# Kernel tuning notes

Hardware: AMD Instinct MI355X
Metric: run time of the kernel (lower is better)

The kernel has to match this reference:

```python
import jax, jax.numpy as jnp
import numpy as np

D_H, HEAD, LAYER_IDX = 1024, 16, 11
D_ATTN = D_H // HEAD
BZ, LEN = 2, 2048


def setup_inputs() -> dict:
    key = jax.random.key(0)
    ks = jax.random.split(key, 8)
    s = 1.0 / np.sqrt(D_H)
    v = jax.random.normal(ks[0], (BZ, LEN, D_H), jnp.float32)
    k = jax.random.normal(ks[1], (BZ, LEN, D_H), jnp.float32)
    q = jax.random.normal(ks[2], (BZ, LEN, D_H), jnp.float32)
    # causal mask: 1.0 where attention is blocked (j > i)
    causal = jnp.triu(jnp.ones((LEN, LEN), jnp.float32), k=1)
    mask = jnp.broadcast_to(causal[None, None], (BZ, 1, LEN, LEN))
    Wv = jax.random.normal(ks[3], (D_H, D_H), jnp.float32) * s
    Wk = jax.random.normal(ks[4], (D_H, D_H), jnp.float32) * s
    Wq = jax.random.normal(ks[5], (D_H, D_H), jnp.float32) * s
    Wo = jax.random.normal(ks[6], (D_H, D_H), jnp.float32) * s
    bo = jnp.zeros((D_H,), jnp.float32)
    return {"v": v, "k": k, "q": q, "mask": mask,
            "Wv": Wv, "Wk": Wk, "Wq": Wq, "Wo": Wo, "bo": bo}


def _split_head(x):
    # (bz, len, d_h) -> (bz, head, len, d_attn)
    bz, L, _ = x.shape
    return x.reshape(bz, L, HEAD, D_ATTN).transpose(0, 2, 1, 3)


def reference(v, k, q, mask, Wv, Wk, Wq, Wo, bo):
    bz, len_q, _ = q.shape
    vh = _split_head(v @ Wv)  # (bz, head, len_k, d_attn)
    kh = _split_head(k @ Wk)
    qh = _split_head(q @ Wq)
    scale = 1.0 / jnp.sqrt(jnp.asarray(D_ATTN, jnp.float32))
    weight = jnp.einsum("bhqd,bhkd->bhqk", qh, kh) * scale
    weight = weight + mask * (-1e9)
    weight = weight / jnp.asarray(LAYER_IDX + 1, jnp.float32)
    attn = jax.nn.softmax(weight, axis=-1)  # dropout omitted (inference)
    out = jnp.einsum("bhqk,bhkd->bhqd", attn, vh)
    out = out.transpose(0, 2, 1, 3).reshape(bz, len_q, D_H)
    return out @ Wo + bo
```

## Files before the change

### kernel.cpp

```cpp
#include <hip/hip_runtime.h>
#include <hip/hip_fp16.h>

typedef _Float16 f16;
typedef _Float16 f16x4 __attribute__((ext_vector_type(4)));
typedef _Float16 f16x8 __attribute__((ext_vector_type(8)));
typedef float f32x4 __attribute__((ext_vector_type(4)));

#define D_H   1024
#define LEN   2048
#define BZ    2
#define NHEAD 16
#define DA    64
#define MTOK  (BZ * LEN)
#define KDIM  1024
#define ATT_SCALE (0.125f / 12.0f)

__device__ __forceinline__ void load_lds16(const f16* g, f16* l) {
  __builtin_amdgcn_global_load_lds((const __attribute__((address_space(1))) void*)g,
                                   (__attribute__((address_space(3))) void*)l,
                                   16, 0, 0);
}

__global__ __launch_bounds__(256)
void k_convert3(const float* __restrict__ q, const float* __restrict__ k,
                const float* __restrict__ v, f16* __restrict__ q16,
                f16* __restrict__ k16, f16* __restrict__ v16) {
  const float* in = (blockIdx.y == 0) ? q : (blockIdx.y == 1) ? k : v;
  f16* out = (blockIdx.y == 0) ? q16 : (blockIdx.y == 1) ? k16 : v16;
  int i = (blockIdx.x * 256 + threadIdx.x) * 4;
  float4 x = *(const float4*)(in + i);
  f16x4 o; o[0] = (f16)x.x; o[1] = (f16)x.y; o[2] = (f16)x.z; o[3] = (f16)x.w;
  *(f16x4*)(out + i) = o;
}

__global__ __launch_bounds__(256)
void k_transpose4(const float* __restrict__ W0, const float* __restrict__ W1,
                  const float* __restrict__ W2, const float* __restrict__ W3,
                  f16* __restrict__ T0, f16* __restrict__ T1,
                  f16* __restrict__ T2, f16* __restrict__ T3) {
  int z = blockIdx.z;
  const float* W = (z == 0) ? W0 : (z == 1) ? W1 : (z == 2) ? W2 : W3;
  f16* Wt = (z == 0) ? T0 : (z == 1) ? T1 : (z == 2) ? T2 : T3;
  __shared__ float tile[32][33];
  int bx = blockIdx.x, by = blockIdx.y;
  int tx = threadIdx.x, ty = threadIdx.y;
#pragma unroll
  for (int s = 0; s < 4; ++s)
    tile[ty + 8 * s][tx] = W[(size_t)(by * 32 + ty + 8 * s) * D_H + bx * 32 + tx];
  __syncthreads();
#pragma unroll
  for (int s = 0; s < 4; ++s)
    Wt[(size_t)(bx * 32 + ty + 8 * s) * D_H + by * 32 + tx] =
        (f16)tile[tx][ty + 8 * s];
}

#define BM 128
#define BN 128
#define BK 64
__device__ __forceinline__ void gemm_core(const f16* __restrict__ A,
                                          const f16* __restrict__ Bt,
                                          f16* As, f16* Bs,
                                          f32x4 (&acc)[4][4]) {
  const int tid = threadIdx.x;
  const int wave = tid >> 6, lane = tid & 63;
  const int lc = lane & 15, quad = lane >> 4;
  const int wm = (wave >> 1) * 64, wn = (wave & 1) * 64;
  const int swz = lc & 7;

  for (int k0 = 0; k0 < KDIM; k0 += BK) {
#pragma unroll
    for (int r = 0; r < 4; ++r) {
      int idx = tid + r * 256;
      int row = idx >> 3, ch = idx & 7;
      int gch = ch ^ (row & 7);
      load_lds16(A + (size_t)row * KDIM + k0 + gch * 8, &As[idx * 8]);
    }
#pragma unroll
    for (int r = 0; r < 4; ++r) {
      int idx = tid + r * 256;
      int row = idx >> 3, ch = idx & 7;
      int gch = ch ^ (row & 7);
      load_lds16(Bt + (size_t)row * KDIM + k0 + gch * 8, &Bs[idx * 8]);
    }
    __syncthreads();
#pragma unroll
    for (int kc = 0; kc < 2; ++kc) {
      f16x8 af[4], bf[4];
#pragma unroll
      for (int mi = 0; mi < 4; ++mi)
        af[mi] = *(const f16x8*)&As[(wm + mi * 16 + lc) * 64 +
                                    (((kc * 4 + quad) ^ swz) * 8)];
#pragma unroll
      for (int ni = 0; ni < 4; ++ni)
        bf[ni] = *(const f16x8*)&Bs[(wn + ni * 16 + lc) * 64 +
                                    (((kc * 4 + quad) ^ swz) * 8)];
#pragma unroll
      for (int mi = 0; mi < 4; ++mi)
#pragma unroll
        for (int ni = 0; ni < 4; ++ni)
          acc[mi][ni] = __builtin_amdgcn_mfma_f32_16x16x32_f16(
              af[mi], bf[ni], acc[mi][ni], 0, 0, 0);
    }
    __syncthreads();
  }
}

__global__ __launch_bounds__(256)
void k_gemm3(const f16* __restrict__ A0, const f16* __restrict__ A1,
             const f16* __restrict__ A2, const f16* __restrict__ W0,
             const f16* __restrict__ W1, const f16* __restrict__ W2,
             f16* __restrict__ O0, f16* __restrict__ O1, f16* __restrict__ O2) {
  __shared__ __align__(16) char smem[(BM + BN) * BK * 2];
  f16* As = (f16*)smem;
  f16* Bs = As + BM * BK;
  const int z = blockIdx.z;
  const f16* A = (z == 0) ? A0 : (z == 1) ? A1 : A2;
  const f16* Bt = (z == 0) ? W0 : (z == 1) ? W1 : W2;
  f16* Out = (z == 0) ? O0 : (z == 1) ? O1 : O2;
  const int m0 = blockIdx.x * BM, n0 = blockIdx.y * BN;
  const int tid = threadIdx.x;
  const int wave = tid >> 6, lane = tid & 63;
  const int lc = lane & 15, quad = lane >> 4;
  const int wm = (wave >> 1) * 64;

  f32x4 acc[4][4] = {};
  gemm_core(A + (size_t)m0 * KDIM, Bt + (size_t)n0 * KDIM, As, Bs, acc);

  if (z <= 1) {
    f16* Ct = (f16*)smem;
#pragma unroll
    for (int hf = 0; hf < 2; ++hf) {
      __syncthreads();
      if ((wave & 1) == hf) {
#pragma unroll
        for (int mi = 0; mi < 4; ++mi)
#pragma unroll
          for (int ni = 0; ni < 4; ++ni)
#pragma unroll
            for (int r = 0; r < 4; ++r) {
              int tok = wm + mi * 16 + quad * 4 + r;
              int d = ni * 16 + lc;
              Ct[tok * 72 + d] = (f16)acc[mi][ni][r];
            }
      }
      __syncthreads();
      int hA = (n0 >> 6) + hf;
#pragma unroll
      for (int it = 0; it < 4; ++it) {
        int u = tid + it * 256;
        int tok = u >> 3, ch = u & 7;
        int gm = m0 + tok;
        int b = gm >> 11, i = gm & 2047;
        f16x8 vv = *(const f16x8*)&Ct[tok * 72 + ch * 8];
        *(f16x8*)(Out + ((size_t)((b << 4) + hA) * LEN + i) * DA + ch * 8) = vv;
      }
    }
  } else {
    f16* Ct = (f16*)smem;
    const int b = m0 >> 11, j0m = m0 & 2047;
#pragma unroll
    for (int hf = 0; hf < 2; ++hf) {
      __syncthreads();
      if ((wave & 1) == hf) {
#pragma unroll
        for (int mi = 0; mi < 4; ++mi)
#pragma unroll
          for (int ni = 0; ni < 4; ++ni)
#pragma unroll
            for (int r = 0; r < 4; ++r) {
              int tok = wm + mi * 16 + quad * 4 + r;
              int d = ni * 16 + lc;
              Ct[d * 136 + tok] = (f16)acc[mi][ni][r];
            }
      }
      __syncthreads();
      int hA = (n0 >> 6) + hf;
#pragma unroll
      for (int it = 0; it < 4; ++it) {
        int u = tid + it * 256;
        int d = u >> 4, ch = u & 15;
        f16x8 vv = *(const f16x8*)&Ct[d * 136 + ch * 8];
        *(f16x8*)(Out + ((size_t)((b << 4) + hA) * DA + d) * LEN + j0m + ch * 8) = vv;
      }
    }
  }
}

#define OM 64
#define ON 128
__global__ __launch_bounds__(256)
void k_gemm_out(const f16* __restrict__ A, const f16* __restrict__ Bt,
                float* __restrict__ Out, const float* __restrict__ bias) {
  __shared__ __align__(16) char smem[(OM + ON) * BK * 2];
  f16* As = (f16*)smem;
  f16* Bs = As + OM * BK;
  const int m0 = blockIdx.x * OM, n0 = blockIdx.y * ON;
  const int tid = threadIdx.x;
  const int wave = tid >> 6, lane = tid & 63;
  const int lc = lane & 15, quad = lane >> 4;
  const int wm = (wave >> 1) * 32, wn = (wave & 1) * 64;
  const int swz = lc & 7;

  f32x4 acc[2][4] = {};

  for (int k0 = 0; k0 < KDIM; k0 += BK) {
#pragma unroll
    for (int r = 0; r < 2; ++r) {
      int idx = tid + r * 256;
      int row = idx >> 3, ch = idx & 7;
      int gch = ch ^ (row & 7);
      load_lds16(A + (size_t)(m0 + row) * KDIM + k0 + gch * 8, &As[idx * 8]);
    }
#pragma unroll
    for (int r = 0; r < 4; ++r) {
      int idx = tid + r * 256;
      int row = idx >> 3, ch = idx & 7;
      int gch = ch ^ (row & 7);
      load_lds16(Bt + (size_t)(n0 + row) * KDIM + k0 + gch * 8, &Bs[idx * 8]);
    }
    __syncthreads();
#pragma unroll
    for (int kc = 0; kc < 2; ++kc) {
      f16x8 af[2], bf[4];
#pragma unroll
      for (int mi = 0; mi < 2; ++mi)
        af[mi] = *(const f16x8*)&As[(wm + mi * 16 + lc) * 64 +
                                    (((kc * 4 + quad) ^ swz) * 8)];
#pragma unroll
      for (int ni = 0; ni < 4; ++ni)
        bf[ni] = *(const f16x8*)&Bs[(wn + ni * 16 + lc) * 64 +
                                    (((kc * 4 + quad) ^ swz) * 8)];
#pragma unroll
      for (int mi = 0; mi < 2; ++mi)
#pragma unroll
        for (int ni = 0; ni < 4; ++ni)
          acc[mi][ni] = __builtin_amdgcn_mfma_f32_16x16x32_f16(
              af[mi], bf[ni], acc[mi][ni], 0, 0, 0);
    }
    __syncthreads();
  }

  float* Ct = (float*)smem;
#pragma unroll
  for (int hf = 0; hf < 2; ++hf) {
    __syncthreads();
    if ((wave & 1) == hf) {
#pragma unroll
      for (int mi = 0; mi < 2; ++mi)
#pragma unroll
        for (int ni = 0; ni < 4; ++ni)
#pragma unroll
          for (int r = 0; r < 4; ++r) {
            int tok = wm + mi * 16 + quad * 4 + r;
            int d = ni * 16 + lc;
            Ct[tok * 68 + d] = acc[mi][ni][r];
          }
    }
    __syncthreads();
#pragma unroll
    for (int it = 0; it < 4; ++it) {
      int u = tid + it * 256;
      int tok = u >> 4, ch = u & 15;
      int gm = m0 + tok;
      int gc = n0 + hf * 64 + ch * 4;
      float4 bv = *(const float4*)(bias + gc);
      float4 cv = *(const float4*)&Ct[tok * 68 + ch * 4];
      float4 ov;
      ov.x = cv.x + bv.x; ov.y = cv.y + bv.y;
      ov.z = cv.z + bv.z; ov.w = cv.w + bv.w;
      *(float4*)(Out + (size_t)gm * D_H + gc) = ov;
    }
  }
}

__global__ __launch_bounds__(256, 4)
void k_attn(const f16* __restrict__ Qh, const f16* __restrict__ Kh,
            const f16* __restrict__ Vt, f16* __restrict__ O16) {
  __shared__ f16 Ks[2][64 * 64];
  __shared__ f16 Vs[2][64 * 64];
  __shared__ f16 Pl[4][16 * 64];
  const int tid = threadIdx.x;
  const int wave = tid >> 6, lane = tid & 63;
  const int lc = lane & 15, quad = lane >> 4;
  const int swz = lc & 7;
  const int bh = blockIdx.x & 31;
  const int qb = 31 - (blockIdx.x >> 5);
  const int i0 = qb * 64 + wave * 16;
  const int b = bh >> 4, h = bh & 15;
  const f16* Qb = Qh + (size_t)bh * LEN * DA;
  const f16* Kb = Kh + (size_t)bh * LEN * DA;
  const f16* Vb = Vt + (size_t)bh * DA * LEN;

  f16x8 aQ[2];
#pragma unroll
  for (int c = 0; c < 2; ++c)
    aQ[c] = *(const f16x8*)(Qb + (size_t)(i0 + lc) * DA + c * 32 + quad * 8);

  float lsum[4] = {0.f, 0.f, 0.f, 0.f};
  f32x4 accO[4] = {};
  f16* P = &Pl[wave][0];

  const int niter = qb + 1;

#pragma unroll
  for (int r = 0; r < 2; ++r) {
    int idx = tid + r * 256;
    int row = idx >> 3, ch = idx & 7;
    int gch = ch ^ (row & 7);
    load_lds16(Kb + (size_t)row * DA + gch * 8, &Ks[0][idx * 8]);
  }
#pragma unroll
  for (int r = 0; r < 2; ++r) {
    int idx = tid + r * 256;
    int row = idx >> 3, ch = idx & 7;
    int gch = ch ^ (row & 7);
    load_lds16(Vb + (size_t)row * LEN + gch * 8, &Vs[0][idx * 8]);
  }

  for (int t = 0; t < niter; ++t) {
    __syncthreads();
    if (t + 1 < niter) {
      int j0n = (t + 1) * 64, nb = (t + 1) & 1;
#pragma unroll
      for (int r = 0; r < 2; ++r) {
        int idx = tid + r * 256;
        int row = idx >> 3, ch = idx & 7;
        int gch = ch ^ (row & 7);
        load_lds16(Kb + (size_t)(j0n + row) * DA + gch * 8, &Ks[nb][idx * 8]);
      }
#pragma unroll
      for (int r = 0; r < 2; ++r) {
        int idx = tid + r * 256;
        int row = idx >> 3, ch = idx & 7;
        int gch = ch ^ (row & 7);
        load_lds16(Vb + (size_t)row * LEN + j0n + gch * 8, &Vs[nb][idx * 8]);
      }
    }
    const f16* ks = Ks[t & 1];
    const f16* vs = Vs[t & 1];

    f32x4 s[4] = {};
#pragma unroll
    for (int g = 0; g < 4; ++g)
#pragma unroll
      for (int c = 0; c < 2; ++c) {
        f16x8 bK = *(const f16x8*)&ks[(g * 16 + lc) * 64 +
                                      (((c * 4 + quad) ^ swz) * 8)];
        s[g] = __builtin_amdgcn_mfma_f32_16x16x32_f16(aQ[c], bK, s[g], 0, 0, 0);
      }
    if (t == niter - 1) {
      const int j0 = t * 64;
#pragma unroll
      for (int g = 0; g < 4; ++g)
#pragma unroll
        for (int r = 0; r < 4; ++r) {
          int row = quad * 4 + r;
          int col = g * 16 + lc;
          float e = __expf(s[g][r] * ATT_SCALE);
          e = (j0 + col > i0 + row) ? 0.f : e;
          lsum[r] += e;
          P[(row * 8 + (((col >> 3)) ^ (row & 7))) * 8 + (col & 7)] = (f16)e;
        }
    } else {
#pragma unroll
      for (int g = 0; g < 4; ++g)
#pragma unroll
        for (int r = 0; r < 4; ++r) {
          int row = quad * 4 + r;
          int col = g * 16 + lc;
          float e = __expf(s[g][r] * ATT_SCALE);
          lsum[r] += e;
          P[(row * 8 + (((col >> 3)) ^ (row & 7))) * 8 + (col & 7)] = (f16)e;
        }
    }
    f16x8 aP0 = *(const f16x8*)&P[(lc * 8 + (quad ^ swz)) * 8];
    f16x8 aP1 = *(const f16x8*)&P[(lc * 8 + ((4 + quad) ^ swz)) * 8];
#pragma unroll
    for (int dc = 0; dc < 4; ++dc) {
      f16x8 bV0 = *(const f16x8*)&vs[(dc * 16 + lc) * 64 + ((quad ^ swz) * 8)];
      f16x8 bV1 = *(const f16x8*)&vs[(dc * 16 + lc) * 64 + (((4 + quad) ^ swz) * 8)];
      accO[dc] = __builtin_amdgcn_mfma_f32_16x16x32_f16(aP0, bV0, accO[dc], 0, 0, 0);
      accO[dc] = __builtin_amdgcn_mfma_f32_16x16x32_f16(aP1, bV1, accO[dc], 0, 0, 0);
    }
  }

#pragma unroll
  for (int off = 1; off < 16; off <<= 1)
#pragma unroll
    for (int r = 0; r < 4; ++r) lsum[r] += __shfl_xor(lsum[r], off, 64);

#pragma unroll
  for (int dc = 0; dc < 4; ++dc)
#pragma unroll
    for (int r = 0; r < 4; ++r) {
      int i = i0 + quad * 4 + r;
      int d = dc * 16 + lc;
      float v = accO[dc][r] / lsum[r];
      O16[((size_t)(b * LEN + i)) * D_H + h * DA + d] = (f16)v;
    }
}

extern "C" void kernel_launch(void* const* d_in, const int* in_sizes, int n_in,
                              void* d_out, int out_size, void* d_ws, size_t ws_size,
                              hipStream_t stream) {
  const float* v_f = (const float*)d_in[0];
  const float* k_f = (const float*)d_in[1];
  const float* q_f = (const float*)d_in[2];
  const float* Wv = (const float*)d_in[4];
  const float* Wk = (const float*)d_in[5];
  const float* Wq = (const float*)d_in[6];
  const float* Wo = (const float*)d_in[7];
  const float* bo = (const float*)d_in[8];
  float* out = (float*)d_out;

  const size_t SZ_X = (size_t)MTOK * D_H;
  const size_t SZ_W = (size_t)D_H * D_H;
  f16* ws = (f16*)d_ws;
  f16* q16 = ws;
  f16* k16 = ws + SZ_X;
  f16* v16 = ws + 2 * SZ_X;
  f16* Qh  = ws + 3 * SZ_X;
  f16* Kh  = ws + 4 * SZ_X;
  f16* Vt  = ws + 5 * SZ_X;
  f16* Wqt = ws + 6 * SZ_X;
  f16* Wkt = Wqt + SZ_W;
  f16* Wvt = Wqt + 2 * SZ_W;
  f16* Wot = Wqt + 3 * SZ_W;
  f16* O16 = q16;

  k_convert3<<<dim3((int)(SZ_X / 1024), 3), 256, 0, stream>>>(q_f, k_f, v_f,
                                                              q16, k16, v16);
  k_transpose4<<<dim3(32, 32, 4), dim3(32, 8), 0, stream>>>(
      Wq, Wk, Wv, Wo, Wqt, Wkt, Wvt, Wot);

  k_gemm3<<<dim3(MTOK / BM, D_H / BN, 3), 256, 0, stream>>>(
      q16, k16, v16, Wqt, Wkt, Wvt, Qh, Kh, Vt);

  k_attn<<<dim3(32 * 32), 256, 0, stream>>>(Qh, Kh, Vt, O16);

  k_gemm_out<<<dim3(MTOK / OM, D_H / ON), 256, 0, stream>>>(O16, Wot, out, bo);
}
```

Measured before the change: 228.9 us.

## Fuse fp32-to-fp16 input conversion into QKV GEMM, double-buffer output GEMM, restructure attention

Drops the separate conversion kernel: the QKV projection GEMM now reads fp32 activations directly and converts them to fp16 while storing into LDS. This removes one launch and an extra write and read of three activation tensors, but the A-tile loads are no longer asynchronous direct-to-LDS. The output projection GEMM gains double-buffered LDS staging so the next K-tile loads while the current one computes. The attention kernel pre-scales Q in fp16, computes the transposed score tile so each lane holds one query's row sum, and writes P as packed f16x4. These steps cut per-element scaling, shuffle reductions and scalar LDS stores.

```diff
diff --git a/kernel.cpp b/kernel.cpp
--- a/kernel.cpp
+++ b/kernel.cpp
@@ -19,18 +19,6 @@
   __builtin_amdgcn_global_load_lds((const __attribute__((address_space(1))) void*)g,
                                    (__attribute__((address_space(3))) void*)l,
                                    16, 0, 0);
-}
-
-__global__ __launch_bounds__(256)
-void k_convert3(const float* __restrict__ q, const float* __restrict__ k,
-                const float* __restrict__ v, f16* __restrict__ q16,
-                f16* __restrict__ k16, f16* __restrict__ v16) {
-  const float* in = (blockIdx.y == 0) ? q : (blockIdx.y == 1) ? k : v;
-  f16* out = (blockIdx.y == 0) ? q16 : (blockIdx.y == 1) ? k16 : v16;
-  int i = (blockIdx.x * 256 + threadIdx.x) * 4;
-  float4 x = *(const float4*)(in + i);
-  f16x4 o; o[0] = (f16)x.x; o[1] = (f16)x.y; o[2] = (f16)x.z; o[3] = (f16)x.w;
-  *(f16x4*)(out + i) = o;
 }
 
 __global__ __launch_bounds__(256)
@@ -57,74 +45,71 @@
 #define BM 128
 #define BN 128
 #define BK 64
-__device__ __forceinline__ void gemm_core(const f16* __restrict__ A,
-                                          const f16* __restrict__ Bt,
-                                          f16* As, f16* Bs,
-                                          f32x4 (&acc)[4][4]) {
-  const int tid = threadIdx.x;
-  const int wave = tid >> 6, lane = tid & 63;
-  const int lc = lane & 15, quad = lane >> 4;
-  const int wm = (wave >> 1) * 64, wn = (wave & 1) * 64;
-  const int swz = lc & 7;
-
-  for (int k0 = 0; k0 < KDIM; k0 += BK) {
-#pragma unroll
-    for (int r = 0; r < 4; ++r) {
-      int idx = tid + r * 256;
-      int row = idx >> 3, ch = idx & 7;
-      int gch = ch ^ (row & 7);
-      load_lds16(A + (size_t)row * KDIM + k0 + gch * 8, &As[idx * 8]);
-    }
-#pragma unroll
-    for (int r = 0; r < 4; ++r) {
-      int idx = tid + r * 256;
-      int row = idx >> 3, ch = idx & 7;
-      int gch = ch ^ (row & 7);
-      load_lds16(Bt + (size_t)row * KDIM + k0 + gch * 8, &Bs[idx * 8]);
-    }
-    __syncthreads();
-#pragma unroll
-    for (int kc = 0; kc < 2; ++kc) {
-      f16x8 af[4], bf[4];
-#pragma unroll
-      for (int mi = 0; mi < 4; ++mi)
-        af[mi] = *(const f16x8*)&As[(wm + mi * 16 + lc) * 64 +
-                                    (((kc * 4 + quad) ^ swz) * 8)];
-#pragma unroll
-      for (int ni = 0; ni < 4; ++ni)
-        bf[ni] = *(const f16x8*)&Bs[(wn + ni * 16 + lc) * 64 +
-                                    (((kc * 4 + quad) ^ swz) * 8)];
-#pragma unroll
-      for (int mi = 0; mi < 4; ++mi)
-#pragma unroll
-        for (int ni = 0; ni < 4; ++ni)
-          acc[mi][ni] = __builtin_amdgcn_mfma_f32_16x16x32_f16(
-              af[mi], bf[ni], acc[mi][ni], 0, 0, 0);
-    }
-    __syncthreads();
-  }
-}
-
 __global__ __launch_bounds__(256)
-void k_gemm3(const f16* __restrict__ A0, const f16* __restrict__ A1,
-             const f16* __restrict__ A2, const f16* __restrict__ W0,
+void k_gemm3(const float* __restrict__ A0, const float* __restrict__ A1,
+             const float* __restrict__ A2, const f16* __restrict__ W0,
              const f16* __restrict__ W1, const f16* __restrict__ W2,
              f16* __restrict__ O0, f16* __restrict__ O1, f16* __restrict__ O2) {
   __shared__ __align__(16) char smem[(BM + BN) * BK * 2];
   f16* As = (f16*)smem;
   f16* Bs = As + BM * BK;
   const int z = blockIdx.z;
-  const f16* A = (z == 0) ? A0 : (z == 1) ? A1 : A2;
+  const float* A = (z == 0) ? A0 : (z == 1) ? A1 : A2;
   const f16* Bt = (z == 0) ? W0 : (z == 1) ? W1 : W2;
   f16* Out = (z == 0) ? O0 : (z == 1) ? O1 : O2;
   const int m0 = blockIdx.x * BM, n0 = blockIdx.y * BN;
   const int tid = threadIdx.x;
   const int wave = tid >> 6, lane = tid & 63;
   const int lc = lane & 15, quad = lane >> 4;
-  const int wm = (wave >> 1) * 64;
+  const int wm = (wave >> 1) * 64, wn = (wave & 1) * 64;
+  const int swz = lc & 7;
+  const float* Ab = A + (size_t)m0 * KDIM;
+  const f16* Bb = Bt + (size_t)n0 * KDIM;
 
   f32x4 acc[4][4] = {};
-  gemm_core(A + (size_t)m0 * KDIM, Bt + (size_t)n0 * KDIM, As, Bs, acc);
+
+  for (int k0 = 0; k0 < KDIM; k0 += BK) {
+#pragma unroll
+    for (int r = 0; r < 4; ++r) {
+      int idx = tid + r * 256;
+      int row = idx >> 3, ch = idx & 7;
+      int gch = ch ^ (row & 7);
+      const float* src = Ab + (size_t)row * KDIM + k0 + gch * 8;
+      float4 x0 = *(const float4*)src;
+      float4 x1 = *(const float4*)(src + 4);
+      f16x8 hh;
+      hh[0] = (f16)x0.x; hh[1] = (f16)x0.y; hh[2] = (f16)x0.z; hh[3] = (f16)x0.w;
+      hh[4] = (f16)x1.x; hh[5] = (f16)x1.y; hh[6] = (f16)x1.z; hh[7] = (f16)x1.w;
+      *(f16x8*)&As[idx * 8] = hh;
+    }
+#pragma unroll
+    for (int r = 0; r < 4; ++r) {
+      int idx = tid + r * 256;
+      int row = idx >> 3, ch = idx & 7;
+      int gch = ch ^ (row & 7);
+      load_lds16(Bb + (size_t)row * KDIM + k0 + gch * 8, &Bs[idx * 8]);
+    }
+    __syncthreads();
+#pragma unroll
+    for (int kc = 0; kc < 2; ++kc) {
+      f16x8 af[4], bf[4];
+#pragma unroll
+      for (int mi = 0; mi < 4; ++mi)
+        af[mi] = *(const f16x8*)&As[(wm + mi * 16 + lc) * 64 +
+                                    (((kc * 4 + quad) ^ swz) * 8)];
+#pragma unroll
+      for (int ni = 0; ni < 4; ++ni)
+        bf[ni] = *(const f16x8*)&Bs[(wn + ni * 16 + lc) * 64 +
+                                    (((kc * 4 + quad) ^ swz) * 8)];
+#pragma unroll
+      for (int mi = 0; mi < 4; ++mi)
+#pragma unroll
+        for (int ni = 0; ni < 4; ++ni)
+          acc[mi][ni] = __builtin_amdgcn_mfma_f32_16x16x32_f16(
+              af[mi], bf[ni], acc[mi][ni], 0, 0, 0);
+    }
+    __syncthreads();
+  }
 
   if (z <= 1) {
     f16* Ct = (f16*)smem;
@@ -188,47 +173,61 @@
 
 #define OM 64
 #define ON 128
+#define ONIT (KDIM / BK)
 __global__ __launch_bounds__(256)
 void k_gemm_out(const f16* __restrict__ A, const f16* __restrict__ Bt,
                 float* __restrict__ Out, const float* __restrict__ bias) {
-  __shared__ __align__(16) char smem[(OM + ON) * BK * 2];
+  __shared__ __align__(16) char smem[2 * (OM + ON) * BK * 2];
   f16* As = (f16*)smem;
-  f16* Bs = As + OM * BK;
+  f16* Bs = As + 2 * OM * BK;
   const int m0 = blockIdx.x * OM, n0 = blockIdx.y * ON;
   const int tid = threadIdx.x;
   const int wave = tid >> 6, lane = tid & 63;
   const int lc = lane & 15, quad = lane >> 4;
   const int wm = (wave >> 1) * 32, wn = (wave & 1) * 64;
   const int swz = lc & 7;
+  const f16* Abase = A + (size_t)m0 * KDIM;
+  const f16* Bbase = Bt + (size_t)n0 * KDIM;
 
   f32x4 acc[2][4] = {};
 
-  for (int k0 = 0; k0 < KDIM; k0 += BK) {
-#pragma unroll
-    for (int r = 0; r < 2; ++r) {
-      int idx = tid + r * 256;
-      int row = idx >> 3, ch = idx & 7;
-      int gch = ch ^ (row & 7);
-      load_lds16(A + (size_t)(m0 + row) * KDIM + k0 + gch * 8, &As[idx * 8]);
-    }
-#pragma unroll
-    for (int r = 0; r < 4; ++r) {
-      int idx = tid + r * 256;
-      int row = idx >> 3, ch = idx & 7;
-      int gch = ch ^ (row & 7);
-      load_lds16(Bt + (size_t)(n0 + row) * KDIM + k0 + gch * 8, &Bs[idx * 8]);
-    }
-    __syncthreads();
+#define STAGE_OUT(t)                                                          \
+  {                                                                           \
+    int k0s = (t) * BK;                                                       \
+    f16* Ad = As + ((t) & 1) * (OM * BK);                                     \
+    f16* Bd = Bs + ((t) & 1) * (ON * BK);                                     \
+    _Pragma("unroll")                                                         \
+    for (int r = 0; r < 2; ++r) {                                             \
+      int idx = tid + r * 256;                                                \
+      int row = idx >> 3, ch = idx & 7;                                       \
+      int gch = ch ^ (row & 7);                                               \
+      load_lds16(Abase + (size_t)row * KDIM + k0s + gch * 8, &Ad[idx * 8]);   \
+    }                                                                         \
+    _Pragma("unroll")                                                         \
+    for (int r = 0; r < 4; ++r) {                                             \
+      int idx = tid + r * 256;                                                \
+      int row = idx >> 3, ch = idx & 7;                                       \
+      int gch = ch ^ (row & 7);                                               \
+      load_lds16(Bbase + (size_t)row * KDIM + k0s + gch * 8, &Bd[idx * 8]);   \
+    }                                                                         \
+  }
+
+  STAGE_OUT(0);
+  for (int t = 0; t < ONIT; ++t) {
+    __syncthreads();
+    if (t + 1 < ONIT) STAGE_OUT(t + 1);
+    const f16* Ad = As + (t & 1) * (OM * BK);
+    const f16* Bd = Bs + (t & 1) * (ON * BK);
 #pragma unroll
     for (int kc = 0; kc < 2; ++kc) {
       f16x8 af[2], bf[4];
 #pragma unroll
       for (int mi = 0; mi < 2; ++mi)
-        af[mi] = *(const f16x8*)&As[(wm + mi * 16 + lc) * 64 +
+        af[mi] = *(const f16x8*)&Ad[(wm + mi * 16 + lc) * 64 +
                                     (((kc * 4 + quad) ^ swz) * 8)];
 #pragma unroll
       for (int ni = 0; ni < 4; ++ni)
-        bf[ni] = *(const f16x8*)&Bs[(wn + ni * 16 + lc) * 64 +
+        bf[ni] = *(const f16x8*)&Bd[(wn + ni * 16 + lc) * 64 +
                                     (((kc * 4 + quad) ^ swz) * 8)];
 #pragma unroll
       for (int mi = 0; mi < 2; ++mi)
@@ -237,7 +236,6 @@
           acc[mi][ni] = __builtin_amdgcn_mfma_f32_16x16x32_f16(
               af[mi], bf[ni], acc[mi][ni], 0, 0, 0);
     }
-    __syncthreads();
   }
 
   float* Ct = (float*)smem;
@@ -278,7 +276,7 @@
             const f16* __restrict__ Vt, f16* __restrict__ O16) {
   __shared__ f16 Ks[2][64 * 64];
   __shared__ f16 Vs[2][64 * 64];
-  __shared__ f16 Pl[4][16 * 64];
+  __shared__ f16 Pw[4][16 * 64];
   const int tid = threadIdx.x;
   const int wave = tid >> 6, lane = tid & 63;
   const int lc = lane & 15, quad = lane >> 4;
@@ -292,13 +290,17 @@
   const f16* Vb = Vt + (size_t)bh * DA * LEN;
 
   f16x8 aQ[2];
-#pragma unroll
-  for (int c = 0; c < 2; ++c)
+  const f16 qs = (f16)ATT_SCALE;
+#pragma unroll
+  for (int c = 0; c < 2; ++c) {
     aQ[c] = *(const f16x8*)(Qb + (size_t)(i0 + lc) * DA + c * 32 + quad * 8);
-
-  float lsum[4] = {0.f, 0.f, 0.f, 0.f};
+#pragma unroll
+    for (int j = 0; j < 8; ++j) aQ[c][j] = aQ[c][j] * qs;
+  }
+
+  float lsum = 0.f;
   f32x4 accO[4] = {};
-  f16* P = &Pl[wave][0];
+  f16* P = &Pw[wave][0];
 
   const int niter = qb + 1;
 
@@ -339,55 +341,67 @@
     const f16* ks = Ks[t & 1];
     const f16* vs = Vs[t & 1];
 
-    f32x4 s[4] = {};
+    f32x4 st[4] = {};
 #pragma unroll
     for (int g = 0; g < 4; ++g)
 #pragma unroll
       for (int c = 0; c < 2; ++c) {
-        f16x8 bK = *(const f16x8*)&ks[(g * 16 + lc) * 64 +
+        f16x8 aK = *(const f16x8*)&ks[(g * 16 + lc) * 64 +
                                       (((c * 4 + quad) ^ swz) * 8)];
-        s[g] = __builtin_amdgcn_mfma_f32_16x16x32_f16(aQ[c], bK, s[g], 0, 0, 0);
-      }
+        st[g] = __builtin_amdgcn_mfma_f32_16x16x32_f16(aK, aQ[c], st[g], 0, 0, 0);
+      }
+    float ev[4][4];
     if (t == niter - 1) {
-      const int j0 = t * 64;
+      const int j0 = t * 64, q = i0 + lc;
 #pragma unroll
       for (int g = 0; g < 4; ++g)
 #pragma unroll
         for (int r = 0; r < 4; ++r) {
-          int row = quad * 4 + r;
-          int col = g * 16 + lc;
-          float e = __expf(s[g][r] * ATT_SCALE);
-          e = (j0 + col > i0 + row) ? 0.f : e;
-          lsum[r] += e;
-          P[(row * 8 + (((col >> 3)) ^ (row & 7))) * 8 + (col & 7)] = (f16)e;
+          int key = j0 + g * 16 + quad * 4 + r;
+          float e = __expf(st[g][r]);
+          e = (key > q) ? 0.f : e;
+          lsum += e;
+          ev[g][r] = e;
         }
     } else {
 #pragma unroll
       for (int g = 0; g < 4; ++g)
 #pragma unroll
         for (int r = 0; r < 4; ++r) {
-          int row = quad * 4 + r;
-          int col = g * 16 + lc;
-          float e = __expf(s[g][r] * ATT_SCALE);
-          lsum[r] += e;
-          P[(row * 8 + (((col >> 3)) ^ (row & 7))) * 8 + (col & 7)] = (f16)e;
+          float e = __expf(st[g][r]);
+          lsum += e;
+          ev[g][r] = e;
         }
     }
-    f16x8 aP0 = *(const f16x8*)&P[(lc * 8 + (quad ^ swz)) * 8];
-    f16x8 aP1 = *(const f16x8*)&P[(lc * 8 + ((4 + quad) ^ swz)) * 8];
+#pragma unroll
+    for (int g = 0; g < 4; ++g) {
+      int c8 = ((g << 1) + (quad >> 1)) ^ swz;
+      f16x4 pk;
+      pk[0] = (f16)ev[g][0]; pk[1] = (f16)ev[g][1];
+      pk[2] = (f16)ev[g][2]; pk[3] = (f16)ev[g][3];
+      *(f16x4*)&P[lc * 64 + c8 * 8 + (quad & 1) * 4] = pk;
+    }
+    __asm__ volatile("s_waitcnt lgkmcnt(0)" ::: "memory");
+    f16x8 aP[2];
+#pragma unroll
+    for (int c = 0; c < 2; ++c) {
+      int c8 = (quad + 4 * c) ^ swz;
+      aP[c] = *(const f16x8*)&P[lc * 64 + c8 * 8];
+    }
 #pragma unroll
     for (int dc = 0; dc < 4; ++dc) {
       f16x8 bV0 = *(const f16x8*)&vs[(dc * 16 + lc) * 64 + ((quad ^ swz) * 8)];
       f16x8 bV1 = *(const f16x8*)&vs[(dc * 16 + lc) * 64 + (((4 + quad) ^ swz) * 8)];
-      accO[dc] = __builtin_amdgcn_mfma_f32_16x16x32_f16(aP0, bV0, accO[dc], 0, 0, 0);
-      accO[dc] = __builtin_amdgcn_mfma_f32_16x16x32_f16(aP1, bV1, accO[dc], 0, 0, 0);
-    }
-  }
-
-#pragma unroll
-  for (int off = 1; off < 16; off <<= 1)
-#pragma unroll
-    for (int r = 0; r < 4; ++r) lsum[r] += __shfl_xor(lsum[r], off, 64);
+      accO[dc] = __builtin_amdgcn_mfma_f32_16x16x32_f16(aP[0], bV0, accO[dc], 0, 0, 0);
+      accO[dc] = __builtin_amdgcn_mfma_f32_16x16x32_f16(aP[1], bV1, accO[dc], 0, 0, 0);
+    }
+  }
+
+  lsum += __shfl_xor(lsum, 16, 64);
+  lsum += __shfl_xor(lsum, 32, 64);
+  float ls[4];
+#pragma unroll
+  for (int r = 0; r < 4; ++r) ls[r] = __shfl(lsum, quad * 4 + r, 64);
 
 #pragma unroll
   for (int dc = 0; dc < 4; ++dc)
@@ -395,7 +409,7 @@
     for (int r = 0; r < 4; ++r) {
       int i = i0 + quad * 4 + r;
       int d = dc * 16 + lc;
-      float v = accO[dc][r] / lsum[r];
+      float v = accO[dc][r] / ls[r];
       O16[((size_t)(b * LEN + i)) * D_H + h * DA + d] = (f16)v;
     }
 }
@@ -416,25 +430,20 @@
   const size_t SZ_X = (size_t)MTOK * D_H;
   const size_t SZ_W = (size_t)D_H * D_H;
   f16* ws = (f16*)d_ws;
-  f16* q16 = ws;
-  f16* k16 = ws + SZ_X;
-  f16* v16 = ws + 2 * SZ_X;
-  f16* Qh  = ws + 3 * SZ_X;
-  f16* Kh  = ws + 4 * SZ_X;
-  f16* Vt  = ws + 5 * SZ_X;
-  f16* Wqt = ws + 6 * SZ_X;
+  f16* Qh  = ws;
+  f16* Kh  = ws + SZ_X;
+  f16* Vt  = ws + 2 * SZ_X;
+  f16* O16 = ws + 3 * SZ_X;
+  f16* Wqt = ws + 4 * SZ_X;
   f16* Wkt = Wqt + SZ_W;
   f16* Wvt = Wqt + 2 * SZ_W;
   f16* Wot = Wqt + 3 * SZ_W;
-  f16* O16 = q16;
-
-  k_convert3<<<dim3((int)(SZ_X / 1024), 3), 256, 0, stream>>>(q_f, k_f, v_f,
-                                                              q16, k16, v16);
+
   k_transpose4<<<dim3(32, 32, 4), dim3(32, 8), 0, stream>>>(
       Wq, Wk, Wv, Wo, Wqt, Wkt, Wvt, Wot);
 
   k_gemm3<<<dim3(MTOK / BM, D_H / BN, 3), 256, 0, stream>>>(
-      q16, k16, v16, Wqt, Wkt, Wvt, Qh, Kh, Vt);
+      q_f, k_f, v_f, Wqt, Wkt, Wvt, Qh, Kh, Vt);
 
   k_attn<<<dim3(32 * 32), 256, 0, stream>>>(Qh, Kh, Vt, O16);
 
```

After: 232.6 us. Within noise of the previous version (+1.6%).
